# Kernel optimization log

Measured on AMD Instinct MI355X. Metric: run time of the kernel, lower is better.

## Reference

```python
import jax, jax.numpy as jnp
import numpy as np

B, SQ, SK, D, DV = 16, 2048, 2048, 64, 64
DROPOUT_P = 0.1


def setup_inputs() -> dict:
    key = jax.random.key(0)
    k1, k2, k3, k4 = jax.random.split(key, 4)
    return {
        "query": jax.random.normal(k1, (B, SQ, D), dtype=jnp.float32),
        "key": jax.random.normal(k2, (B, SK, D), dtype=jnp.float32),
        "value": jax.random.normal(k3, (B, SK, DV), dtype=jnp.float32),
        "drop_mask": jax.random.uniform(k4, (B, SQ, SK), dtype=jnp.float32),
    }


def reference(query, key, value, drop_mask):
    # scaled dot-product attention with explicit score matrix, as in the module
    scale = jnp.sqrt(jnp.asarray(key.shape[-1], dtype=query.dtype))
    qk = jnp.einsum("bqd,bkd->bqk", query, key) / scale  # [B, SQ, SK]
    attn = jax.nn.softmax(qk, axis=-1)
    # dropout: keep where uniform > p, rescale by 1/(1-p)
    keep = (drop_mask > DROPOUT_P).astype(attn.dtype)
    attn = attn * keep / (1.0 - DROPOUT_P)
    return jnp.einsum("bqk,bkv->bqv", attn, value)  # [B, SQ, DV]
```

## Files before the change

### kernel.cpp

```cpp
#include <hip/hip_runtime.h>
#include <hip/hip_bf16.h>

#define B_ 16
#define SQ_ 2048
#define SK_ 2048
#define D_ 64
#define DV_ 64
#define INV_KEEP 1.1111111f
#define QSCALE 0.1803368801f

typedef float f4 __attribute__((ext_vector_type(4)));
typedef __bf16 bf16x2 __attribute__((ext_vector_type(2)));
typedef __bf16 bf16x8 __attribute__((ext_vector_type(8)));
typedef short s16x4 __attribute__((ext_vector_type(4)));
typedef unsigned int u32;
typedef unsigned int u32x2 __attribute__((ext_vector_type(2)));
typedef unsigned int u32x4 __attribute__((ext_vector_type(4)));

static __device__ __forceinline__ unsigned short bf16u(float f) {
    u32 u = __builtin_bit_cast(u32, f);
    u += 0x7fffu + ((u >> 16) & 1u);
    return (unsigned short)(u >> 16);
}
static __device__ __forceinline__ u32 pk2(float lo, float hi) {
    return (u32)bf16u(lo) | ((u32)bf16u(hi) << 16);
}
static __device__ __forceinline__ u32 pkc(float lo, float hi) {
    bf16x2 t = {(__bf16)lo, (__bf16)hi};
    return __builtin_bit_cast(u32, t);
}

static __device__ __forceinline__ float fexp2(float x) {
#if __has_builtin(__builtin_amdgcn_exp2f)
    return __builtin_amdgcn_exp2f(x);
#else
    return exp2f(x);
#endif
}

static __device__ __forceinline__ void gload16(const void* g, void* l) {
    __builtin_amdgcn_global_load_lds(
        (const __attribute__((address_space(1))) unsigned int*)g,
        (__attribute__((address_space(3))) unsigned int*)l, 16, 0, 0);
}

template <int OFF>
static __device__ __forceinline__ f4 gload_f4(const float* p) {
    f4 d;
    if constexpr (OFF == 0)
        asm volatile("global_load_dwordx4 %0, %1, off" : "=v"(d) : "v"(p));
    else
        asm volatile("global_load_dwordx4 %0, %1, off offset:%2" : "=v"(d) : "v"(p), "i"(OFF));
    return d;
}

static __device__ __forceinline__ f4 mfma16(s16x4 a, s16x4 b, f4 c) {
#if __has_builtin(__builtin_amdgcn_mfma_f32_16x16x16bf16_1k)
    return __builtin_amdgcn_mfma_f32_16x16x16bf16_1k(a, b, c, 0, 0, 0);
#else
    f4 d;
    asm("v_mfma_f32_16x16x16_bf16 %0, %1, %2, %3" : "=v"(d) : "v"(a), "v"(b), "v"(c));
    return d;
#endif
}

__global__ __launch_bounds__(256) void kv_retile(const float* __restrict__ K,
                                                 const float* __restrict__ V,
                                                 unsigned short* __restrict__ KbT,
                                                 unsigned short* __restrict__ VtT) {
    if (blockIdx.x < 1024) {
        int b = blockIdx.x >> 6, kt = blockIdx.x & 63;
        int p = threadIdx.x;
        int s = p >> 6, g = (p >> 4) & 3, c = p & 15;
        int t = s & 1, h = s >> 1;
        const float* src = K + ((size_t)(b * SK_ + kt * 32 + 16 * t + c)) * D_ + 32 * h + 8 * g;
        f4 a = *(const f4*)src;
        f4 b2 = *(const f4*)(src + 4);
        u32x4 w;
        w[0] = pk2(a.x, a.y); w[1] = pk2(a.z, a.w);
        w[2] = pk2(b2.x, b2.y); w[3] = pk2(b2.z, b2.w);
        *(u32x4*)(KbT + ((size_t)(b * 64 + kt)) * 2048 + (size_t)p * 8) = w;
    } else {
        __shared__ float vt[32][65];
        int id = blockIdx.x - 1024;
        int b = id >> 6, kt = id & 63;
        int tid = threadIdx.x;
#pragma unroll
        for (int e = 0; e < 2; ++e) {
            int f = tid * 2 + e;
            int row = f >> 4, c4 = (f & 15) * 4;
            *(f4*)&vt[row][c4] = *(const f4*)(V + ((size_t)(b * SK_ + kt * 32 + row)) * DV_ + c4);
        }
        __syncthreads();
        int vb = tid >> 6, g = (tid >> 4) & 3, c = tid & 15;
        int v = vb * 16 + c;
        u32x4 w;
        w[0] = pk2(vt[4 * g + 0][v], vt[4 * g + 1][v]);
        w[1] = pk2(vt[4 * g + 2][v], vt[4 * g + 3][v]);
        w[2] = pk2(vt[16 + 4 * g + 0][v], vt[16 + 4 * g + 1][v]);
        w[3] = pk2(vt[16 + 4 * g + 2][v], vt[16 + 4 * g + 3][v]);
        *(u32x4*)(VtT + ((size_t)(b * 64 + kt)) * 2048 + (size_t)tid * 8) = w;
    }
}

template <int SPLIT>
__global__ __launch_bounds__(256) void attn_main(const float* __restrict__ Q,
                                                 const unsigned short* __restrict__ KbT,
                                                 const unsigned short* __restrict__ VtT,
                                                 const float* __restrict__ mask,
                                                 float* __restrict__ out,
                                                 float* __restrict__ accP,
                                                 float* __restrict__ lP) {
    constexpr int NT32 = SK_ / SPLIT / 32;
    constexpr int NB = 512 * SPLIT;
    __shared__ unsigned short sK[4][2048];
    __shared__ unsigned short sV[4][2048];

    int bswz = (blockIdx.x & 7) * (NB / 8) + (blockIdx.x >> 3);
    int wid  = threadIdx.x >> 6;
    int split = bswz & (SPLIT - 1);
    int strip = (bswz / SPLIT) * 4 + wid;
    int b  = strip >> 7;
    int q0 = (strip & 127) << 4;
    int kb = split * (SK_ / SPLIT);
    int lane = threadIdx.x & 63;
    int g = lane >> 4, c = lane & 15;

    const size_t tile0 = ((size_t)b * 64 + split * NT32) * 2048;
    const unsigned short* ksrc = KbT + tile0 + (size_t)threadIdx.x * 8;
    const unsigned short* vsrc = VtT + tile0 + (size_t)threadIdx.x * 8;
    const float* msrc = mask + ((size_t)(b * SQ_ + q0 + c)) * SK_ + kb + 4 * g;

    bf16x8 qf[2];
    {
        const float* qp = Q + ((size_t)(b * SQ_ + q0 + c)) * D_ + 8 * g;
#pragma unroll
        for (int h = 0; h < 2; ++h) {
            f4 a  = *(const f4*)(qp + h * 32);
            f4 bq = *(const f4*)(qp + h * 32 + 4);
            u32x4 wq;
            wq[0] = pk2(a.x * QSCALE, a.y * QSCALE);
            wq[1] = pk2(a.z * QSCALE, a.w * QSCALE);
            wq[2] = pk2(bq.x * QSCALE, bq.y * QSCALE);
            wq[3] = pk2(bq.z * QSCALE, bq.w * QSCALE);
            qf[h] = __builtin_bit_cast(bf16x8, wq);
        }
    }
    __builtin_amdgcn_sched_barrier(0);

    f4 mreg[4][2];

    auto kvload = [&](int dst, int srct) {
        gload16(ksrc + (size_t)srct * 2048, &sK[dst][wid * 512]);
        gload16(vsrc + (size_t)srct * 2048, &sV[dst][wid * 512]);
    };
    auto mload = [&](int dst, int srct) {
        const float* mp = msrc + (size_t)srct * 32;
        mreg[dst][0] = gload_f4<0>(mp);
        mreg[dst][1] = gload_f4<64>(mp);
    };

    mload(0, 0);
    mload(1, 1);
    kvload(0, 0);
    kvload(1, 1);
    kvload(2, 2);

    f4 acc[4];
#pragma unroll
    for (int vb = 0; vb < 4; ++vb) acc[vb] = (f4){0.f, 0.f, 0.f, 0.f};
    f4 ls0 = (f4){0.f, 0.f, 0.f, 0.f}, ls1 = (f4){0.f, 0.f, 0.f, 0.f};

    const unsigned short* kbL = &sK[0][0] + lane * 8;
    const unsigned short* vbL = &sV[0][0] + lane * 8;

#pragma unroll 4
    for (int kt = 0; kt < NT32; ++kt) {
        if ((kt & 1) == 0)
            asm volatile("s_waitcnt vmcnt(4)" ::: "memory");
        else
            asm volatile("s_waitcnt vmcnt(8)" ::: "memory");
        __builtin_amdgcn_s_barrier();
        __builtin_amdgcn_sched_barrier(0);

        kvload((kt + 3) & 3, (kt + 3 < NT32) ? kt + 3 : NT32 - 1);
        if ((kt & 1) == 0) {
            const int mt = (kt + 2 < NT32) ? kt + 2 : NT32 - 2;
            const float* mp = msrc + (size_t)mt * 32;
            mreg[(kt + 2) & 3][0] = gload_f4<0>(mp);
            mreg[(kt + 2) & 3][1] = gload_f4<64>(mp);
            mreg[(kt + 3) & 3][0] = gload_f4<128>(mp);
            mreg[(kt + 3) & 3][1] = gload_f4<192>(mp);
        }

        const int bi = kt & 3;
        const unsigned short* kB = kbL + bi * 2048;
        const unsigned short* vB = vbL + bi * 2048;

        u32x4 ka0 = *(const u32x4*)(kB);
        u32x4 ka1 = *(const u32x4*)(kB + 1024);
        u32x4 kc0 = *(const u32x4*)(kB + 512);
        u32x4 kc1 = *(const u32x4*)(kB + 1536);
        f4 st0 = (f4){0.f, 0.f, 0.f, 0.f}, st1 = (f4){0.f, 0.f, 0.f, 0.f};
        st0 = __builtin_amdgcn_mfma_f32_16x16x32_bf16(__builtin_bit_cast(bf16x8, ka0), qf[0], st0, 0, 0, 0);
        st0 = __builtin_amdgcn_mfma_f32_16x16x32_bf16(__builtin_bit_cast(bf16x8, ka1), qf[1], st0, 0, 0, 0);
        st1 = __builtin_amdgcn_mfma_f32_16x16x32_bf16(__builtin_bit_cast(bf16x8, kc0), qf[0], st1, 0, 0, 0);
        st1 = __builtin_amdgcn_mfma_f32_16x16x32_bf16(__builtin_bit_cast(bf16x8, kc1), qf[1], st1, 0, 0, 0);

        const f4 mk0 = mreg[bi][0], mk1 = mreg[bi][1];
        float pd0[4], pd1[4];
#pragma unroll
        for (int r = 0; r < 4; ++r) {
            float p0 = fexp2(st0[r]);
            ls0[r] += p0;
            pd0[r] = (mk0[r] > 0.1f) ? p0 : 0.f;
            float p1 = fexp2(st1[r]);
            ls1[r] += p1;
            pd1[r] = (mk1[r] > 0.1f) ? p1 : 0.f;
        }

        u32x2 pw0, pw1;
        pw0[0] = pkc(pd0[0], pd0[1]); pw0[1] = pkc(pd0[2], pd0[3]);
        pw1[0] = pkc(pd1[0], pd1[1]); pw1[1] = pkc(pd1[2], pd1[3]);
        s16x4 pb0 = __builtin_bit_cast(s16x4, pw0);
        s16x4 pb1 = __builtin_bit_cast(s16x4, pw1);
#pragma unroll
        for (int vb = 0; vb < 4; ++vb) {
            u32x4 vv = *(const u32x4*)(vB + vb * 512);
            u32x2 vlo, vhi;
            vlo[0] = vv[0]; vlo[1] = vv[1];
            vhi[0] = vv[2]; vhi[1] = vv[3];
            acc[vb] = mfma16(__builtin_bit_cast(s16x4, vlo), pb0, acc[vb]);
            acc[vb] = mfma16(__builtin_bit_cast(s16x4, vhi), pb1, acc[vb]);
        }
    }
    asm volatile("s_waitcnt vmcnt(0)" ::: "memory");

    float lf = ls0[0] + ls0[1] + ls0[2] + ls0[3] + ls1[0] + ls1[1] + ls1[2] + ls1[3];
    lf += __shfl_xor(lf, 16);
    lf += __shfl_xor(lf, 32);

    if constexpr (SPLIT == 1) {
        float li = INV_KEEP / lf;
        float* op = out + ((size_t)(b * SQ_ + q0 + c)) * DV_;
#pragma unroll
        for (int vb = 0; vb < 4; ++vb) {
            f4 o = acc[vb] * li;
            __builtin_nontemporal_store(o, (f4*)(op + 16 * vb + 4 * g));
        }
    } else {
        float* ap = accP + (((size_t)strip * SPLIT + split) * 64 + lane) * 16;
#pragma unroll
        for (int vb = 0; vb < 4; ++vb)
            *(f4*)(ap + 4 * vb) = acc[vb];
        if (g == 0)
            lP[((size_t)strip * SPLIT + split) * 16 + c] = lf;
    }
}

__global__ __launch_bounds__(256) void attn_combine2(const float* __restrict__ accP,
                                                     const float* __restrict__ lP,
                                                     float* __restrict__ out) {
    __shared__ float sacc[2 * 1280];
    __shared__ float sl[32];
    int strip = blockIdx.x;
    int t = threadIdx.x;
    const float* src = accP + (size_t)strip * 2048;
#pragma unroll
    for (int s = 0; s < 2; ++s)
        *(f4*)&sacc[s * 1280 + (t >> 2) * 20 + (t & 3) * 4] = *(const f4*)(src + s * 1024 + t * 4);
    if (t < 32) sl[t] = lP[(size_t)strip * 32 + t];
    __syncthreads();

    int q = t >> 4, j = t & 15;
    float L = sl[q] + sl[16 + q];
    float inv = INV_KEEP / L;
    int base = (16 * (j & 3) + q) * 20 + 4 * (j >> 2);
    f4 o = *(const f4*)&sacc[base] + *(const f4*)&sacc[1280 + base];
    o *= inv;
    int b  = strip >> 7;
    int q0 = (strip & 127) << 4;
    __builtin_nontemporal_store(o, (f4*)(out + ((size_t)(b * SQ_ + q0 + q)) * DV_ + 4 * j));
}

extern "C" void kernel_launch(void* const* d_in, const int* in_sizes, int n_in,
                              void* d_out, int out_size, void* d_ws, size_t ws_size,
                              hipStream_t stream) {
    const float* Q = (const float*)d_in[0];
    const float* K = (const float*)d_in[1];
    const float* V = (const float*)d_in[2];
    const float* M = (const float*)d_in[3];
    float* out = (float*)d_out;

    char* ws = (char*)d_ws;
    unsigned short* KbT  = (unsigned short*)ws;
    unsigned short* VtT  = (unsigned short*)(ws + (size_t)4 * 1024 * 1024);
    float*          accP = (float*)         (ws + (size_t)8 * 1024 * 1024);
    float*          lP   = (float*)         (ws + (size_t)24 * 1024 * 1024);

    const size_t need_split = (size_t)24 * 1024 * 1024 + (size_t)2048 * 2 * 16 * 4;

    kv_retile<<<2048, 256, 0, stream>>>(K, V, KbT, VtT);
    if (ws_size >= need_split) {
        attn_main<2><<<1024, 256, 0, stream>>>(Q, KbT, VtT, M, out, accP, lP);
        attn_combine2<<<2048, 256, 0, stream>>>(accP, lP, out);
    } else {
        attn_main<1><<<512, 256, 0, stream>>>(Q, KbT, VtT, M, out, nullptr, nullptr);
    }
}
```

Baseline: 90.43 us.

## Precompute dropout mask as bitfield in prep kernel and read bits in attention

```diff
diff --git a/kernel.cpp b/kernel.cpp
--- a/kernel.cpp
+++ b/kernel.cpp
@@ -42,16 +42,6 @@
     __builtin_amdgcn_global_load_lds(
         (const __attribute__((address_space(1))) unsigned int*)g,
         (__attribute__((address_space(3))) unsigned int*)l, 16, 0, 0);
-}
-
-template <int OFF>
-static __device__ __forceinline__ f4 gload_f4(const float* p) {
-    f4 d;
-    if constexpr (OFF == 0)
-        asm volatile("global_load_dwordx4 %0, %1, off" : "=v"(d) : "v"(p));
-    else
-        asm volatile("global_load_dwordx4 %0, %1, off offset:%2" : "=v"(d) : "v"(p), "i"(OFF));
-    return d;
 }
 
 static __device__ __forceinline__ f4 mfma16(s16x4 a, s16x4 b, f4 c) {
@@ -64,10 +54,13 @@
 #endif
 }
 
-__global__ __launch_bounds__(256) void kv_retile(const float* __restrict__ K,
-                                                 const float* __restrict__ V,
-                                                 unsigned short* __restrict__ KbT,
-                                                 unsigned short* __restrict__ VtT) {
+__global__ __launch_bounds__(256) void prep_all(const float* __restrict__ K,
+                                                const float* __restrict__ V,
+                                                const float* __restrict__ mask,
+                                                unsigned short* __restrict__ KbT,
+                                                unsigned short* __restrict__ VtT,
+                                                u32* __restrict__ bits) {
+    __shared__ float vt[32][65];
     if (blockIdx.x < 1024) {
         int b = blockIdx.x >> 6, kt = blockIdx.x & 63;
         int p = threadIdx.x;
@@ -80,8 +73,7 @@
         w[0] = pk2(a.x, a.y); w[1] = pk2(a.z, a.w);
         w[2] = pk2(b2.x, b2.y); w[3] = pk2(b2.z, b2.w);
         *(u32x4*)(KbT + ((size_t)(b * 64 + kt)) * 2048 + (size_t)p * 8) = w;
-    } else {
-        __shared__ float vt[32][65];
+    } else if (blockIdx.x < 2048) {
         int id = blockIdx.x - 1024;
         int b = id >> 6, kt = id & 63;
         int tid = threadIdx.x;
@@ -100,6 +92,35 @@
         w[2] = pk2(vt[16 + 4 * g + 0][v], vt[16 + 4 * g + 1][v]);
         w[3] = pk2(vt[16 + 4 * g + 2][v], vt[16 + 4 * g + 3][v]);
         *(u32x4*)(VtT + ((size_t)(b * 64 + kt)) * 2048 + (size_t)tid * 8) = w;
+    } else {
+        int strip = blockIdx.x - 2048;
+        int b  = strip >> 7;
+        int q0 = (strip & 127) << 4;
+        int w    = threadIdx.x >> 6;
+        int lane = threadIdx.x & 63;
+        int g = lane >> 4, c = lane & 15;
+        const float* mrow = mask + ((size_t)(b * SQ_ + q0 + c)) * SK_ + 4 * g;
+        u32x4 outw;
+#pragma unroll
+        for (int tgl = 0; tgl < 4; ++tgl) {
+            int tg = w * 4 + tgl;
+            u32 word = 0;
+#pragma unroll
+            for (int ti = 0; ti < 4; ++ti) {
+                const float* p = mrow + tg * 128 + ti * 32;
+                f4 lo = *(const f4*)(p);
+                f4 hi = *(const f4*)(p + 16);
+                u32 by = 0;
+#pragma unroll
+                for (int r = 0; r < 4; ++r) {
+                    by |= (lo[r] > 0.1f ? (1u << r) : 0u);
+                    by |= (hi[r] > 0.1f ? (1u << (4 + r)) : 0u);
+                }
+                word |= by << (8 * ti);
+            }
+            outw[tgl] = word;
+        }
+        *(u32x4*)(bits + ((size_t)strip * 64 + lane) * 16 + w * 4) = outw;
     }
 }
 
@@ -107,12 +128,13 @@
 __global__ __launch_bounds__(256) void attn_main(const float* __restrict__ Q,
                                                  const unsigned short* __restrict__ KbT,
                                                  const unsigned short* __restrict__ VtT,
-                                                 const float* __restrict__ mask,
+                                                 const u32* __restrict__ bits,
                                                  float* __restrict__ out,
                                                  float* __restrict__ accP,
                                                  float* __restrict__ lP) {
     constexpr int NT32 = SK_ / SPLIT / 32;
     constexpr int NB = 512 * SPLIT;
+    constexpr int NWORDS = NT32 / 4;
     __shared__ unsigned short sK[4][2048];
     __shared__ unsigned short sV[4][2048];
 
@@ -122,14 +144,20 @@
     int strip = (bswz / SPLIT) * 4 + wid;
     int b  = strip >> 7;
     int q0 = (strip & 127) << 4;
-    int kb = split * (SK_ / SPLIT);
     int lane = threadIdx.x & 63;
     int g = lane >> 4, c = lane & 15;
 
     const size_t tile0 = ((size_t)b * 64 + split * NT32) * 2048;
     const unsigned short* ksrc = KbT + tile0 + (size_t)threadIdx.x * 8;
     const unsigned short* vsrc = VtT + tile0 + (size_t)threadIdx.x * 8;
-    const float* msrc = mask + ((size_t)(b * SQ_ + q0 + c)) * SK_ + kb + 4 * g;
+
+    u32 bw[NWORDS];
+    {
+        const u32* bbase = bits + ((size_t)strip * 64 + lane) * 16 + split * NWORDS;
+#pragma unroll
+        for (int n = 0; n < NWORDS / 4; ++n)
+            *(u32x4*)&bw[n * 4] = *(const u32x4*)(bbase + n * 4);
+    }
 
     bf16x8 qf[2];
     {
@@ -148,20 +176,11 @@
     }
     __builtin_amdgcn_sched_barrier(0);
 
-    f4 mreg[4][2];
-
     auto kvload = [&](int dst, int srct) {
         gload16(ksrc + (size_t)srct * 2048, &sK[dst][wid * 512]);
         gload16(vsrc + (size_t)srct * 2048, &sV[dst][wid * 512]);
     };
-    auto mload = [&](int dst, int srct) {
-        const float* mp = msrc + (size_t)srct * 32;
-        mreg[dst][0] = gload_f4<0>(mp);
-        mreg[dst][1] = gload_f4<64>(mp);
-    };
-
-    mload(0, 0);
-    mload(1, 1);
+
     kvload(0, 0);
     kvload(1, 1);
     kvload(2, 2);
@@ -174,28 +193,18 @@
     const unsigned short* kbL = &sK[0][0] + lane * 8;
     const unsigned short* vbL = &sV[0][0] + lane * 8;
 
-#pragma unroll 4
+#pragma unroll
     for (int kt = 0; kt < NT32; ++kt) {
-        if ((kt & 1) == 0)
-            asm volatile("s_waitcnt vmcnt(4)" ::: "memory");
-        else
-            asm volatile("s_waitcnt vmcnt(8)" ::: "memory");
+        asm volatile("s_waitcnt vmcnt(4)" ::: "memory");
         __builtin_amdgcn_s_barrier();
         __builtin_amdgcn_sched_barrier(0);
 
         kvload((kt + 3) & 3, (kt + 3 < NT32) ? kt + 3 : NT32 - 1);
-        if ((kt & 1) == 0) {
-            const int mt = (kt + 2 < NT32) ? kt + 2 : NT32 - 2;
-            const float* mp = msrc + (size_t)mt * 32;
-            mreg[(kt + 2) & 3][0] = gload_f4<0>(mp);
-            mreg[(kt + 2) & 3][1] = gload_f4<64>(mp);
-            mreg[(kt + 3) & 3][0] = gload_f4<128>(mp);
-            mreg[(kt + 3) & 3][1] = gload_f4<192>(mp);
-        }
 
         const int bi = kt & 3;
         const unsigned short* kB = kbL + bi * 2048;
         const unsigned short* vB = vbL + bi * 2048;
+        const u32 mby = (bw[kt >> 2] >> ((kt & 3) * 8)) & 0xFFu;
 
         u32x4 ka0 = *(const u32x4*)(kB);
         u32x4 ka1 = *(const u32x4*)(kB + 1024);
@@ -207,16 +216,15 @@
         st1 = __builtin_amdgcn_mfma_f32_16x16x32_bf16(__builtin_bit_cast(bf16x8, kc0), qf[0], st1, 0, 0, 0);
         st1 = __builtin_amdgcn_mfma_f32_16x16x32_bf16(__builtin_bit_cast(bf16x8, kc1), qf[1], st1, 0, 0, 0);
 
-        const f4 mk0 = mreg[bi][0], mk1 = mreg[bi][1];
         float pd0[4], pd1[4];
 #pragma unroll
         for (int r = 0; r < 4; ++r) {
             float p0 = fexp2(st0[r]);
             ls0[r] += p0;
-            pd0[r] = (mk0[r] > 0.1f) ? p0 : 0.f;
+            pd0[r] = (mby & (1u << r)) ? p0 : 0.f;
             float p1 = fexp2(st1[r]);
             ls1[r] += p1;
-            pd1[r] = (mk1[r] > 0.1f) ? p1 : 0.f;
+            pd1[r] = (mby & (1u << (4 + r))) ? p1 : 0.f;
         }
 
         u32x2 pw0, pw1;
@@ -294,17 +302,18 @@
 
     char* ws = (char*)d_ws;
     unsigned short* KbT  = (unsigned short*)ws;
-    unsigned short* VtT  = (unsigned short*)(ws + (size_t)4 * 1024 * 1024);
-    float*          accP = (float*)         (ws + (size_t)8 * 1024 * 1024);
-    float*          lP   = (float*)         (ws + (size_t)24 * 1024 * 1024);
-
-    const size_t need_split = (size_t)24 * 1024 * 1024 + (size_t)2048 * 2 * 16 * 4;
-
-    kv_retile<<<2048, 256, 0, stream>>>(K, V, KbT, VtT);
+    unsigned short* VtT  = (unsigned short*)(ws + (size_t)4  * 1024 * 1024);
+    u32*            bits = (u32*)           (ws + (size_t)8  * 1024 * 1024);
+    float*          accP = (float*)         (ws + (size_t)16 * 1024 * 1024);
+    float*          lP   = (float*)         (ws + (size_t)32 * 1024 * 1024);
+
+    const size_t need_split = (size_t)32 * 1024 * 1024 + (size_t)2048 * 2 * 16 * 4;
+
+    prep_all<<<4096, 256, 0, stream>>>(K, V, M, KbT, VtT, bits);
     if (ws_size >= need_split) {
-        attn_main<2><<<1024, 256, 0, stream>>>(Q, KbT, VtT, M, out, accP, lP);
+        attn_main<2><<<1024, 256, 0, stream>>>(Q, KbT, VtT, bits, out, accP, lP);
         attn_combine2<<<2048, 256, 0, stream>>>(accP, lP, out);
     } else {
-        attn_main<1><<<512, 256, 0, stream>>>(Q, KbT, VtT, M, out, nullptr, nullptr);
-    }
-}
+        attn_main<1><<<512, 256, 0, stream>>>(Q, KbT, VtT, bits, out, nullptr, nullptr);
+    }
+}
```

Measured after the change: 98.68 us. 9.1% more time.
